# Performance work log

Hardware: AMD Instinct MI355X
Metric: run time of the kernel (lower is better)

## Reference

```python
import jax, jax.numpy as jnp
import numpy as np

N_NODES = 100000
N_EDGES = 1600000


def gcn_conv(x, W, b, src, dst, n):
    # PyG GCNConv: x @ W, add self-loops, symmetric deg^{-1/2} normalization,
    # sum-aggregate messages from src into dst, then add bias.
    h = x @ W  # [N, out]
    loops = jnp.arange(n, dtype=src.dtype)
    s = jnp.concatenate([src, loops])
    d = jnp.concatenate([dst, loops])
    deg = jax.ops.segment_sum(jnp.ones_like(d, dtype=h.dtype), d, num_segments=n)
    dinv = 1.0 / jnp.sqrt(deg)  # deg >= 1 thanks to self-loops
    norm = dinv[s] * dinv[d]  # [E + N]
    msg = h[s] * norm[:, None]
    out = jax.ops.segment_sum(msg, d, num_segments=n)
    return out + b


def setup_inputs() -> dict:
    key = jax.random.key(0)
    k1, k2, k3, k4 = jax.random.split(key, 4)
    x = jax.random.normal(k1, (N_NODES, 64), dtype=jnp.float32)
    edge_index = jax.random.randint(k2, (2, N_EDGES), 0, N_NODES, dtype=jnp.int64)
    W1 = jax.random.normal(k3, (64, 32), dtype=jnp.float32) * (1.0 / np.sqrt(64))
    b1 = jnp.zeros((32,), dtype=jnp.float32)
    W2 = jax.random.normal(k4, (32, 16), dtype=jnp.float32) * (1.0 / np.sqrt(32))
    b2 = jnp.zeros((16,), dtype=jnp.float32)
    return {"x": x, "edge_index": edge_index, "W1": W1, "b1": b1, "W2": W2, "b2": b2}


def reference(x, edge_index, W1, b1, W2, b2):
    n = x.shape[0]
    src, dst = edge_index[0], edge_index[1]
    h = gcn_conv(x, W1, b1, src, dst, n)
    h = jax.nn.relu(h)
    h = gcn_conv(h, W2, b2, src, dst, n)
    return jax.nn.log_softmax(h, axis=1)
```

## Files before the change

### kernel.cpp

```cpp
#include <hip/hip_runtime.h>
#include <hip/hip_bf16.h>


#define FEAT_IN 64
#define FEAT_H  32
#define FEAT_O  16
#define MAXNB   512
#define PART_G  256
#define CAP     5120

__device__ __forceinline__ float2 upk_bf2(unsigned w) {
    return make_float2(__uint_as_float(w << 16), __uint_as_float(w & 0xFFFF0000u));
}

__global__ void k_part1(const int* __restrict__ src, const int* __restrict__ dst, int e,
                        int* __restrict__ gcur, int* __restrict__ part, int G, int NBk) {
    __shared__ int lh[MAXNB];
    __shared__ int rb[MAXNB];
    int t = threadIdx.x, g = blockIdx.x;
    for (int i = t; i < NBk; i += 256) lh[i] = 0;
    __syncthreads();
    int chunk = (e + G - 1) / G;
    int beg = g * chunk, end = min(e, beg + chunk);
    for (int i = beg + t; i < end; i += 256) atomicAdd(&lh[dst[i] >> 8], 1);
    __syncthreads();
    for (int i = t; i < NBk; i += 256) {
        int c = lh[i];
        rb[i] = c ? atomicAdd(&gcur[i], c) : 0;
    }
    __syncthreads();
    for (int i = t; i < NBk; i += 256) lh[i] = i * CAP + rb[i];
    __syncthreads();
    for (int i = beg + t; i < end; i += 256) {
        int s_ = src[i], d_ = dst[i];
        int pos = atomicAdd(&lh[d_ >> 8], 1);
        part[pos] = s_ | ((d_ & 255) << 24);
    }
}

__global__ void k_csr_gemm1(const int* __restrict__ part, const int* __restrict__ gcur,
                            int NBk, int n,
                            const float* __restrict__ x, const float* __restrict__ W1,
                            int2* __restrict__ row_info, int* __restrict__ col,
                            __hip_bfloat162* __restrict__ h1s2) {
    __shared__ int cnt[256], spre[256], cur[256], ssc[256];
    __shared__ float sdv[256];
    __shared__ float sW[FEAT_IN * FEAT_H];
    __shared__ float sx[16][FEAT_IN + 1];
    int t = threadIdx.x, b = blockIdx.x;
    int beg = b * CAP;
    int end = beg + gcur[b];
    cnt[t] = 0;
    for (int i = t; i < FEAT_IN * FEAT_H; i += 256) sW[i] = W1[i];
    __syncthreads();
    for (int j = beg + t; j < end; j += 256) atomicAdd(&cnt[((unsigned)part[j]) >> 24], 1);
    __syncthreads();
    int v = cnt[t];
    ssc[t] = v;
    __syncthreads();
    for (int off = 1; off < 256; off <<= 1) {
        int xv = (t >= off) ? ssc[t - off] : 0;
        __syncthreads();
        ssc[t] += xv;
        __syncthreads();
    }
    spre[t] = ssc[t] - v;
    sdv[t] = rsqrtf((float)v + 1.0f);
    int node = b * 256 + t;
    if (node < n) row_info[node] = make_int2(beg + spre[t], v);
    cur[t] = beg + spre[t];
    __syncthreads();
    for (int j = beg + t; j < end; j += 256) {
        int r = part[j];
        int dl = ((unsigned)r) >> 24;
        int off = atomicAdd(&cur[dl], 1);
        col[off] = r & 0x00FFFFFF;
    }
#pragma unroll 1
    for (int tile = 0; tile < 16; ++tile) {
        int nodeBase = b * 256 + tile * 16;
        __syncthreads();
        {
            int xn = t >> 4, c = t & 15;
            int nd = nodeBase + xn;
            if (nd < n) {
                float4 vv = ((const float4*)x)[(size_t)nd * 16 + c];
                sx[xn][c * 4 + 0] = vv.x; sx[xn][c * 4 + 1] = vv.y;
                sx[xn][c * 4 + 2] = vv.z; sx[xn][c * 4 + 3] = vv.w;
            }
        }
        __syncthreads();
        int nl = t >> 4, gg = t & 15;
        int nd = nodeBase + nl;
        if (nd < n) {
            float a0 = 0.0f, a1 = 0.0f;
#pragma unroll
            for (int k = 0; k < FEAT_IN; ++k) {
                float s = sx[nl][k];
                a0 += s * sW[k * FEAT_H + 2 * gg];
                a1 += s * sW[k * FEAT_H + 2 * gg + 1];
            }
            float dvn = sdv[tile * 16 + nl];
            __hip_bfloat162 o;
            o.x = __float2bfloat16(a0 * dvn);
            o.y = __float2bfloat16(a1 * dvn);
            h1s2[(size_t)nd * 16 + gg] = o;
        }
    }
}

__global__ void k_gather1_gemm2(const int2* __restrict__ row_info, const int* __restrict__ col,
                                const uint4* __restrict__ h1q, const float* __restrict__ W2,
                                const float* __restrict__ b1,
                                __hip_bfloat162* __restrict__ h2s2, int n) {
    __shared__ float sW[FEAT_H * FEAT_O];
    __shared__ float sb1[FEAT_H];
    __shared__ float sz[64][FEAT_H + 1];
    __shared__ float sdv[64];
    int t = threadIdx.x;
    for (int i = t; i < FEAT_H * FEAT_O; i += 256) sW[i] = W2[i];
    if (t < FEAT_H) sb1[t] = b1[t];
    __syncthreads();

    int g = t >> 2, l = t & 3;
    int d = blockIdx.x * 64 + g;
    if (d < n) {
        float a[8];
        {
            uint4 u = h1q[(size_t)d * 4 + l];
            float2 p;
            p = upk_bf2(u.x); a[0] = p.x; a[1] = p.y;
            p = upk_bf2(u.y); a[2] = p.x; a[3] = p.y;
            p = upk_bf2(u.z); a[4] = p.x; a[5] = p.y;
            p = upk_bf2(u.w); a[6] = p.x; a[7] = p.y;
        }
        int2 ri = row_info[d];
        int beg = ri.x, end = ri.x + ri.y;
        int j = beg;
        for (; j + 4 <= end; j += 4) {
            int c0 = col[j + 0], c1 = col[j + 1], c2 = col[j + 2], c3 = col[j + 3];
            uint4 u0 = h1q[(size_t)c0 * 4 + l];
            uint4 u1 = h1q[(size_t)c1 * 4 + l];
            uint4 u2 = h1q[(size_t)c2 * 4 + l];
            uint4 u3 = h1q[(size_t)c3 * 4 + l];
            float2 p;
            p = upk_bf2(u0.x); a[0] += p.x; a[1] += p.y;
            p = upk_bf2(u0.y); a[2] += p.x; a[3] += p.y;
            p = upk_bf2(u0.z); a[4] += p.x; a[5] += p.y;
            p = upk_bf2(u0.w); a[6] += p.x; a[7] += p.y;
            p = upk_bf2(u1.x); a[0] += p.x; a[1] += p.y;
            p = upk_bf2(u1.y); a[2] += p.x; a[3] += p.y;
            p = upk_bf2(u1.z); a[4] += p.x; a[5] += p.y;
            p = upk_bf2(u1.w); a[6] += p.x; a[7] += p.y;
            p = upk_bf2(u2.x); a[0] += p.x; a[1] += p.y;
            p = upk_bf2(u2.y); a[2] += p.x; a[3] += p.y;
            p = upk_bf2(u2.z); a[4] += p.x; a[5] += p.y;
            p = upk_bf2(u2.w); a[6] += p.x; a[7] += p.y;
            p = upk_bf2(u3.x); a[0] += p.x; a[1] += p.y;
            p = upk_bf2(u3.y); a[2] += p.x; a[3] += p.y;
            p = upk_bf2(u3.z); a[4] += p.x; a[5] += p.y;
            p = upk_bf2(u3.w); a[6] += p.x; a[7] += p.y;
        }
        for (; j < end; ++j) {
            uint4 u = h1q[(size_t)col[j] * 4 + l];
            float2 p;
            p = upk_bf2(u.x); a[0] += p.x; a[1] += p.y;
            p = upk_bf2(u.y); a[2] += p.x; a[3] += p.y;
            p = upk_bf2(u.z); a[4] += p.x; a[5] += p.y;
            p = upk_bf2(u.w); a[6] += p.x; a[7] += p.y;
        }
        float dv = rsqrtf((float)ri.y + 1.0f);
        if (l == 0) sdv[g] = dv;
#pragma unroll
        for (int k = 0; k < 8; ++k)
            sz[g][l * 8 + k] = fmaxf(dv * a[k] + sb1[l * 8 + k], 0.0f);
    }
    __syncthreads();
#pragma unroll
    for (int it = 0; it < 2; ++it) {
        int nl = (t >> 3) + it * 32;
        int m = t & 7;
        int node = blockIdx.x * 64 + nl;
        if (node < n) {
            float a0 = 0.0f, a1 = 0.0f;
#pragma unroll
            for (int f = 0; f < FEAT_H; ++f) {
                float z = sz[nl][f];
                a0 += z * sW[f * FEAT_O + 2 * m];
                a1 += z * sW[f * FEAT_O + 2 * m + 1];
            }
            float dv = sdv[nl];
            __hip_bfloat162 o;
            o.x = __float2bfloat16(a0 * dv);
            o.y = __float2bfloat16(a1 * dv);
            h2s2[(size_t)node * 8 + m] = o;
        }
    }
}

__global__ void k_gather2_lsm(const int2* __restrict__ row_info, const int* __restrict__ col,
                              const uint4* __restrict__ h2q, const float* __restrict__ b2,
                              float4* __restrict__ out4, int n) {
    __shared__ float sb2[FEAT_O];
    int t = threadIdx.x;
    if (t < FEAT_O) sb2[t] = b2[t];
    __syncthreads();
    int g = t >> 1, h = t & 1;
    int d = blockIdx.x * 128 + g;
    if (d >= n) return;
    float a[8];
    {
        uint4 u = h2q[(size_t)d * 2 + h];
        float2 p;
        p = upk_bf2(u.x); a[0] = p.x; a[1] = p.y;
        p = upk_bf2(u.y); a[2] = p.x; a[3] = p.y;
        p = upk_bf2(u.z); a[4] = p.x; a[5] = p.y;
        p = upk_bf2(u.w); a[6] = p.x; a[7] = p.y;
    }
    int2 ri = row_info[d];
    int beg = ri.x, end = ri.x + ri.y;
    int j = beg;
    for (; j + 4 <= end; j += 4) {
        int c0 = col[j + 0], c1 = col[j + 1], c2 = col[j + 2], c3 = col[j + 3];
        uint4 u0 = h2q[(size_t)c0 * 2 + h];
        uint4 u1 = h2q[(size_t)c1 * 2 + h];
        uint4 u2 = h2q[(size_t)c2 * 2 + h];
        uint4 u3 = h2q[(size_t)c3 * 2 + h];
        float2 p;
        p = upk_bf2(u0.x); a[0] += p.x; a[1] += p.y;
        p = upk_bf2(u0.y); a[2] += p.x; a[3] += p.y;
        p = upk_bf2(u0.z); a[4] += p.x; a[5] += p.y;
        p = upk_bf2(u0.w); a[6] += p.x; a[7] += p.y;
        p = upk_bf2(u1.x); a[0] += p.x; a[1] += p.y;
        p = upk_bf2(u1.y); a[2] += p.x; a[3] += p.y;
        p = upk_bf2(u1.z); a[4] += p.x; a[5] += p.y;
        p = upk_bf2(u1.w); a[6] += p.x; a[7] += p.y;
        p = upk_bf2(u2.x); a[0] += p.x; a[1] += p.y;
        p = upk_bf2(u2.y); a[2] += p.x; a[3] += p.y;
        p = upk_bf2(u2.z); a[4] += p.x; a[5] += p.y;
        p = upk_bf2(u2.w); a[6] += p.x; a[7] += p.y;
        p = upk_bf2(u3.x); a[0] += p.x; a[1] += p.y;
        p = upk_bf2(u3.y); a[2] += p.x; a[3] += p.y;
        p = upk_bf2(u3.z); a[4] += p.x; a[5] += p.y;
        p = upk_bf2(u3.w); a[6] += p.x; a[7] += p.y;
    }
    for (; j < end; ++j) {
        uint4 u = h2q[(size_t)col[j] * 2 + h];
        float2 p;
        p = upk_bf2(u.x); a[0] += p.x; a[1] += p.y;
        p = upk_bf2(u.y); a[2] += p.x; a[3] += p.y;
        p = upk_bf2(u.z); a[4] += p.x; a[5] += p.y;
        p = upk_bf2(u.w); a[6] += p.x; a[7] += p.y;
    }
    float dv = rsqrtf((float)ri.y + 1.0f);
    float v[8];
    float mx = -1e30f;
#pragma unroll
    for (int k = 0; k < 8; ++k) {
        v[k] = dv * a[k] + sb2[h * 8 + k];
        mx = fmaxf(mx, v[k]);
    }
    mx = fmaxf(mx, __shfl_xor(mx, 1));
    float ssum = 0.0f;
#pragma unroll
    for (int k = 0; k < 8; ++k) ssum += __expf(v[k] - mx);
    ssum += __shfl_xor(ssum, 1);
    float lg = mx + logf(ssum);
    float4 o0 = { v[0] - lg, v[1] - lg, v[2] - lg, v[3] - lg };
    float4 o1 = { v[4] - lg, v[5] - lg, v[6] - lg, v[7] - lg };
    out4[(size_t)d * 4 + h * 2 + 0] = o0;
    out4[(size_t)d * 4 + h * 2 + 1] = o1;
}

extern "C" void kernel_launch(void* const* d_in, const int* in_sizes, int n_in,
                              void* d_out, int out_size, void* d_ws, size_t ws_size,
                              hipStream_t stream) {
    const float* x  = (const float*)d_in[0];
    const int*   ei = (const int*)d_in[1];
    const float* W1 = (const float*)d_in[2];
    const float* b1 = (const float*)d_in[3];
    const float* W2 = (const float*)d_in[4];
    const float* b2 = (const float*)d_in[5];

    const int n = in_sizes[0] / FEAT_IN;
    const int e = in_sizes[1] / 2;
    const int* src = ei;
    const int* dst = ei + e;
    const int NBk = (n + 255) >> 8;
    const int G = PART_G;

    int*  gcur = (int*)d_ws;
    int*  part = gcur + MAXNB;
    int*  col  = part + (size_t)NBk * CAP;
    int2* row_info = (int2*)(col + (size_t)NBk * CAP);
    __hip_bfloat162* h1s2 = (__hip_bfloat162*)(row_info + n);
    __hip_bfloat162* h2s2 = h1s2 + 16 * (size_t)n;

    hipMemsetAsync(gcur, 0, (size_t)NBk * sizeof(int), stream);
    k_part1<<<G, 256, 0, stream>>>(src, dst, e, gcur, part, G, NBk);
    k_csr_gemm1<<<NBk, 256, 0, stream>>>(part, gcur, NBk, n, x, W1, row_info, col, h1s2);
    k_gather1_gemm2<<<(n + 63) / 64, 256, 0, stream>>>(row_info, col, (const uint4*)h1s2,
                                                       W2, b1, h2s2, n);
    k_gather2_lsm<<<(n + 127) / 128, 256, 0, stream>>>(row_info, col, (const uint4*)h2s2,
                                                       b2, (float4*)d_out, n);
}
```

Baseline: 189.0 us.

## Split CSR build and first GEMM into separate kernels for more parallelism

New measurement: 184.5 us. -2.3%, faster.

```diff
diff --git a/kernel.cpp b/kernel.cpp
--- a/kernel.cpp
+++ b/kernel.cpp
@@ -38,20 +38,13 @@
     }
 }
 
-__global__ void k_csr_gemm1(const int* __restrict__ part, const int* __restrict__ gcur,
-                            int NBk, int n,
-                            const float* __restrict__ x, const float* __restrict__ W1,
-                            int2* __restrict__ row_info, int* __restrict__ col,
-                            __hip_bfloat162* __restrict__ h1s2) {
+__global__ void k_csr(const int* __restrict__ part, const int* __restrict__ gcur,
+                      int NBk, int n, int2* __restrict__ row_info, int* __restrict__ col) {
     __shared__ int cnt[256], spre[256], cur[256], ssc[256];
-    __shared__ float sdv[256];
-    __shared__ float sW[FEAT_IN * FEAT_H];
-    __shared__ float sx[16][FEAT_IN + 1];
     int t = threadIdx.x, b = blockIdx.x;
     int beg = b * CAP;
     int end = beg + gcur[b];
     cnt[t] = 0;
-    for (int i = t; i < FEAT_IN * FEAT_H; i += 256) sW[i] = W1[i];
     __syncthreads();
     for (int j = beg + t; j < end; j += 256) atomicAdd(&cnt[((unsigned)part[j]) >> 24], 1);
     __syncthreads();
@@ -65,7 +58,6 @@
         __syncthreads();
     }
     spre[t] = ssc[t] - v;
-    sdv[t] = rsqrtf((float)v + 1.0f);
     int node = b * 256 + t;
     if (node < n) row_info[node] = make_int2(beg + spre[t], v);
     cur[t] = beg + spre[t];
@@ -76,35 +68,44 @@
         int off = atomicAdd(&cur[dl], 1);
         col[off] = r & 0x00FFFFFF;
     }
-#pragma unroll 1
-    for (int tile = 0; tile < 16; ++tile) {
-        int nodeBase = b * 256 + tile * 16;
+}
+
+__global__ void k_gemm1(const float* __restrict__ x, const float* __restrict__ W1,
+                        const int2* __restrict__ row_info,
+                        __hip_bfloat162* __restrict__ h1s2, int n) {
+    __shared__ float sW[FEAT_IN * FEAT_H];
+    __shared__ float sx[16][FEAT_IN + 1];
+    int t = threadIdx.x;
+    for (int i = t; i < FEAT_IN * FEAT_H; i += 256) sW[i] = W1[i];
+#pragma unroll
+    for (int tile = 0; tile < 2; ++tile) {
+        int nodeBase = blockIdx.x * 32 + tile * 16;
         __syncthreads();
         {
             int xn = t >> 4, c = t & 15;
-            int nd = nodeBase + xn;
-            if (nd < n) {
-                float4 vv = ((const float4*)x)[(size_t)nd * 16 + c];
-                sx[xn][c * 4 + 0] = vv.x; sx[xn][c * 4 + 1] = vv.y;
-                sx[xn][c * 4 + 2] = vv.z; sx[xn][c * 4 + 3] = vv.w;
+            int node = nodeBase + xn;
+            if (node < n) {
+                float4 v = ((const float4*)x)[(size_t)node * 16 + c];
+                sx[xn][c * 4 + 0] = v.x; sx[xn][c * 4 + 1] = v.y;
+                sx[xn][c * 4 + 2] = v.z; sx[xn][c * 4 + 3] = v.w;
             }
         }
         __syncthreads();
-        int nl = t >> 4, gg = t & 15;
-        int nd = nodeBase + nl;
-        if (nd < n) {
+        int nl = t >> 4, g = t & 15;
+        int node = nodeBase + nl;
+        if (node < n) {
             float a0 = 0.0f, a1 = 0.0f;
 #pragma unroll
             for (int k = 0; k < FEAT_IN; ++k) {
                 float s = sx[nl][k];
-                a0 += s * sW[k * FEAT_H + 2 * gg];
-                a1 += s * sW[k * FEAT_H + 2 * gg + 1];
+                a0 += s * sW[k * FEAT_H + 2 * g];
+                a1 += s * sW[k * FEAT_H + 2 * g + 1];
             }
-            float dvn = sdv[tile * 16 + nl];
+            float dv = rsqrtf((float)row_info[node].y + 1.0f);
             __hip_bfloat162 o;
-            o.x = __float2bfloat16(a0 * dvn);
-            o.y = __float2bfloat16(a1 * dvn);
-            h1s2[(size_t)nd * 16 + gg] = o;
+            o.x = __float2bfloat16(a0 * dv);
+            o.y = __float2bfloat16(a1 * dv);
+            h1s2[(size_t)node * 16 + g] = o;
         }
     }
 }
@@ -298,7 +299,8 @@
 
     hipMemsetAsync(gcur, 0, (size_t)NBk * sizeof(int), stream);
     k_part1<<<G, 256, 0, stream>>>(src, dst, e, gcur, part, G, NBk);
-    k_csr_gemm1<<<NBk, 256, 0, stream>>>(part, gcur, NBk, n, x, W1, row_info, col, h1s2);
+    k_csr<<<NBk, 256, 0, stream>>>(part, gcur, NBk, n, row_info, col);
+    k_gemm1<<<(n + 31) / 32, 256, 0, stream>>>(x, W1, row_info, h1s2, n);
     k_gather1_gemm2<<<(n + 63) / 64, 256, 0, stream>>>(row_info, col, (const uint4*)h1s2,
                                                        W2, b1, h2s2, n);
     k_gather2_lsm<<<(n + 127) / 128, 256, 0, stream>>>(row_info, col, (const uint4*)h2s2,
```
